# Optimization experiments

Measured on AMD Instinct MI355X. Metric: run time of the kernel, lower is better.

## Reference

```python
import jax, jax.numpy as jnp
import numpy as np

NEG_SLOPE = 0.01  # torch F.leaky_relu default

N_NODES = 100000
N_EDGES = 1250000
N_REL = 10
D = 64


def setup_inputs() -> dict:
    key = jax.random.key(0)
    ks = jax.random.split(key, 8)
    return {
        "nfeat": jax.random.normal(ks[0], (N_NODES, D), dtype=jnp.float32),
        "efeat": jax.random.normal(ks[1], (N_EDGES, D), dtype=jnp.float32),
        "relation_weight": jax.random.normal(ks[2], (N_REL, D, D), dtype=jnp.float32) * (1.0 / np.sqrt(D)),
        "res_fc_w": jax.random.normal(ks[3], (D, D), dtype=jnp.float32) * (1.0 / np.sqrt(D)),
        "res_fc2_w": jax.random.normal(ks[4], (D, D), dtype=jnp.float32) * (1.0 / np.sqrt(D)),
        "src": jax.random.randint(ks[5], (N_EDGES,), 0, N_NODES, dtype=jnp.int32),
        "dst": jnp.sort(jax.random.randint(ks[6], (N_EDGES,), 0, N_NODES, dtype=jnp.int32)),
        "etype": jax.random.randint(ks[7], (N_EDGES,), 0, N_REL, dtype=jnp.int32),
    }


def reference(nfeat, efeat, relation_weight, res_fc_w, res_fc2_w, src, dst, etype):
    # KGAT conv (eval mode, feat_drop=0):
    #   t_r = W_{r(e)} h_src,  h_r = W_{r(e)} h_dst
    #   att = <t_r, tanh(h_r + e_r)>  per edge
    #   a   = edge_softmax over incoming edges of dst
    #   h_neighbor[v] = sum_{e: dst=v} a_e * h_src
    #   h' = leaky_relu((h + h_nb) W1^T) + leaky_relu((h * h_nb) W2^T)
    n = nfeat.shape[0]
    # Project every node by every relation once (N*R*D), instead of
    # materializing a per-edge [E, D, D] weight gather.
    proj = jnp.einsum('ni,rio->nro', nfeat, relation_weight)  # [N, R, D]
    t_r = proj[src, etype]   # [E, D]
    h_r = proj[dst, etype]   # [E, D]
    att = jnp.sum(t_r * jnp.tanh(h_r + efeat), axis=-1)  # [E]

    # segment softmax over dst (edge_softmax)
    seg_max = jax.ops.segment_max(att, dst, num_segments=n)  # [N]
    ex = jnp.exp(att - seg_max[dst])
    seg_sum = jax.ops.segment_sum(ex, dst, num_segments=n)   # [N]
    a = ex / seg_sum[dst]                                    # [E]

    # weighted scatter-sum aggregation of src features
    h_nb = jax.ops.segment_sum(nfeat[src] * a[:, None], dst, num_segments=n)  # [N, D]

    out = (jax.nn.leaky_relu((nfeat + h_nb) @ res_fc_w.T, NEG_SLOPE)
           + jax.nn.leaky_relu((nfeat * h_nb) @ res_fc2_w.T, NEG_SLOPE))
    return out
```

## Files before the change

### kernel.cpp

```cpp
#include <hip/hip_runtime.h>
#include <hip/hip_fp16.h>
#include <math.h>

#define D 64
#define WAVE 64

typedef _Float16 f16;
typedef f16 f16x8 __attribute__((ext_vector_type(8)));
typedef float f32x4 __attribute__((ext_vector_type(4)));

__device__ __forceinline__ float wave_reduce_sum(float v) {
    v += __shfl_xor(v, 32);
    v += __shfl_xor(v, 16);
    v += __shfl_xor(v, 8);
    v += __shfl_xor(v, 4);
    v += __shfl_xor(v, 2);
    v += __shfl_xor(v, 1);
    return v;
}

__device__ __forceinline__ float wave_reduce_max(float v) {
    v = fmaxf(v, __shfl_xor(v, 32));
    v = fmaxf(v, __shfl_xor(v, 16));
    v = fmaxf(v, __shfl_xor(v, 8));
    v = fmaxf(v, __shfl_xor(v, 4));
    v = fmaxf(v, __shfl_xor(v, 2));
    v = fmaxf(v, __shfl_xor(v, 1));
    return v;
}

__device__ __forceinline__ float fast_tanh(float x) {
    float e = __expf(2.0f * x);
    return 1.0f - 2.0f / (e + 1.0f);
}

__global__ void wt_kernel(const float* __restrict__ W, f16* __restrict__ WT,
                          int n_rel) {
    int idx = blockIdx.x * blockDim.x + threadIdx.x;
    if (idx >= n_rel * D * D) return;
    int r = idx >> 12;
    int rem = idx & 4095;
    int o = rem >> 6;
    int k = rem & 63;
    WT[idx] = (f16)W[((size_t)r << 12) + (k << 6) + o];
}

__global__ __launch_bounds__(256) void proj_kernel(
    const float* __restrict__ nfeat, const f16* __restrict__ WT,
    f16* __restrict__ proj, int n_nodes, int n_rel) {
    __shared__ f16 Al[64 * D];
    const int tid = threadIdx.x;
    const int lane = tid & 63;
    const int wid = tid >> 6;
    const int n0 = blockIdx.x * 64;

    {
        const float4* g4 = (const float4*)(nfeat + (size_t)n0 * D);
        int avail_rows = n_nodes - n0;
        if (avail_rows > 64) avail_rows = 64;
        const int avail4 = avail_rows * (D / 4);
#pragma unroll
        for (int i = tid; i < 64 * (D / 4); i += 256) {
            float4 v = (i < avail4) ? g4[i] : make_float4(0.f, 0.f, 0.f, 0.f);
            f16* dp = &Al[i * 4];
            dp[0] = (f16)v.x; dp[1] = (f16)v.y; dp[2] = (f16)v.z; dp[3] = (f16)v.w;
        }
    }
    __syncthreads();

    const int g = lane >> 4;
    const int c = lane & 15;
    const int arow = wid * 16 + c;
    f16x8 a0 = *(const f16x8*)&Al[arow * D + g * 8];
    f16x8 a1 = *(const f16x8*)&Al[arow * D + 32 + g * 8];

    const int row_base = n0 + wid * 16 + g * 4;

    for (int r = 0; r < n_rel; ++r) {
        const f16* Wb = WT + ((size_t)r << 12);
        f32x4 acc[4] = {{0.f,0.f,0.f,0.f},{0.f,0.f,0.f,0.f},
                        {0.f,0.f,0.f,0.f},{0.f,0.f,0.f,0.f}};
#pragma unroll
        for (int t = 0; t < 4; ++t) {
            const f16* bp = Wb + (size_t)(t * 16 + c) * D + g * 8;
            f16x8 b0 = *(const f16x8*)bp;
            f16x8 b1 = *(const f16x8*)(bp + 32);
            acc[t] = __builtin_amdgcn_mfma_f32_16x16x32_f16(a0, b0, acc[t], 0, 0, 0);
            acc[t] = __builtin_amdgcn_mfma_f32_16x16x32_f16(a1, b1, acc[t], 0, 0, 0);
        }
#pragma unroll
        for (int t = 0; t < 4; ++t) {
#pragma unroll
            for (int j = 0; j < 4; ++j) {
                int n = row_base + j;
                if (n < n_nodes)
                    proj[((size_t)n * n_rel + r) * D + t * 16 + c] = (f16)acc[t][j];
            }
        }
    }
}

__global__ __launch_bounds__(256) void att_kernel(
    const __half* __restrict__ proj, const float* __restrict__ efeat,
    const int* __restrict__ src, const int* __restrict__ dst,
    const int* __restrict__ etype, float* __restrict__ att,
    int n_edges, int n_rel) {
    const int lane = threadIdx.x & 63;
    const int wid = threadIdx.x >> 6;
    const int g = lane >> 4;
    const int c4 = lane & 15;

    int e = (blockIdx.x * 4 + wid) * 4 + g;
    const bool valid = e < n_edges;
    const int ec = valid ? e : (n_edges - 1);
    const int s = src[ec];
    const int d = dst[ec];
    const int et = etype[ec];

    const float4* ef4 = (const float4*)(efeat + (size_t)ec * D);
    float4 ef = ef4[c4];
    const __half2* tp = (const __half2*)(proj + ((size_t)s * n_rel + et) * D) + c4 * 2;
    const __half2* hp = (const __half2*)(proj + ((size_t)d * n_rel + et) * D) + c4 * 2;
    float2 tA = __half22float2(tp[0]);
    float2 tB = __half22float2(tp[1]);
    float2 hA = __half22float2(hp[0]);
    float2 hB = __half22float2(hp[1]);

    float v = tA.x * fast_tanh(hA.x + ef.x)
            + tA.y * fast_tanh(hA.y + ef.y)
            + tB.x * fast_tanh(hB.x + ef.z)
            + tB.y * fast_tanh(hB.y + ef.w);
    v += __shfl_xor(v, 8);
    v += __shfl_xor(v, 4);
    v += __shfl_xor(v, 2);
    v += __shfl_xor(v, 1);
    if (valid && c4 == 0) att[e] = v;
}

__global__ void rowptr_kernel(const int* __restrict__ dst, int* __restrict__ row_ptr,
                              int n_edges, int n_nodes) {
    int tid = blockIdx.x * blockDim.x + threadIdx.x;
    int stride = gridDim.x * blockDim.x;
    for (int e = tid; e < n_edges; e += stride) {
        int d = dst[e];
        int dprev = (e == 0) ? -1 : dst[e - 1];
        for (int v = dprev + 1; v <= d; ++v) row_ptr[v] = e;
    }
    if (tid == 0) {
        int dlast = dst[n_edges - 1];
        for (int v = dlast + 1; v <= n_nodes; ++v) row_ptr[v] = n_edges;
    }
}

__global__ __launch_bounds__(256) void agg_kernel(
    const float* __restrict__ att, const int* __restrict__ src,
    const int* __restrict__ row_ptr, const float* __restrict__ nfeat,
    float* __restrict__ h_nb, int n_nodes) {
    const int lane = threadIdx.x & 63;
    const int wid = __builtin_amdgcn_readfirstlane(threadIdx.x >> 6);
    const int n = blockIdx.x * 4 + wid;
    if (n >= n_nodes) return;
    const int s = row_ptr[n];
    const int t = row_ptr[n + 1];
    float a0 = 0.0f, a1 = 0.0f, a2 = 0.0f, a3 = 0.0f;
    float inv = 0.0f;
    if (t > s) {
        float m = -INFINITY;
        for (int base = s; base < t; base += WAVE) {
            int idx = base + lane;
            float a = (idx < t) ? att[idx] : -INFINITY;
            m = fmaxf(m, a);
        }
        m = wave_reduce_max(m);
        float exsum = 0.0f;
        for (int base = s; base < t; base += WAVE) {
            int idx = base + lane;
            float ex = (idx < t) ? __expf(att[idx] - m) : 0.0f;
            int sv = (idx < t) ? src[idx] : 0;
            exsum += ex;
            int cnt = t - base;
            if (cnt > WAVE) cnt = WAVE;
            int cnt4 = (cnt + 3) & ~3;
            for (int j = 0; j < cnt4; j += 4) {
                float c0 = __shfl(ex, j + 0); int s0 = __shfl(sv, j + 0);
                float c1 = __shfl(ex, j + 1); int s1 = __shfl(sv, j + 1);
                float c2 = __shfl(ex, j + 2); int s2 = __shfl(sv, j + 2);
                float c3 = __shfl(ex, j + 3); int s3 = __shfl(sv, j + 3);
                a0 = fmaf(c0, nfeat[(size_t)s0 * D + lane], a0);
                a1 = fmaf(c1, nfeat[(size_t)s1 * D + lane], a1);
                a2 = fmaf(c2, nfeat[(size_t)s2 * D + lane], a2);
                a3 = fmaf(c3, nfeat[(size_t)s3 * D + lane], a3);
            }
        }
        float ssum = wave_reduce_sum(exsum);
        inv = 1.0f / ssum;
    }
    h_nb[(size_t)n * D + lane] = ((a0 + a1) + (a2 + a3)) * inv;
}

__global__ __launch_bounds__(256) void out_kernel(
    const float* __restrict__ nfeat, const float* h_nb,
    const float* __restrict__ W1, const float* __restrict__ W2,
    float* out, int n_nodes) {
    const int lane = threadIdx.x & 63;
    const int wid = __builtin_amdgcn_readfirstlane(threadIdx.x >> 6);
    float w1[D], w2[D];
#pragma unroll
    for (int i = 0; i < D; ++i) w1[i] = W1[lane * D + i];
#pragma unroll
    for (int i = 0; i < D; ++i) w2[i] = W2[lane * D + i];
    const int nwaves = gridDim.x * 4;
    for (int n = blockIdx.x * 4 + wid; n < n_nodes; n += nwaves) {
        const int nn = __builtin_amdgcn_readfirstlane(n);
        const float* x = nfeat + (size_t)nn * D;
        const float* h = h_nb + (size_t)nn * D;
        float a0 = 0.0f, a1 = 0.0f, b0 = 0.0f, b1 = 0.0f;
#pragma unroll
        for (int i = 0; i < D; i += 2) {
            float x0 = x[i], h0 = h[i];
            float x1 = x[i + 1], h1 = h[i + 1];
            a0 = fmaf(x0 + h0, w1[i], a0);
            b0 = fmaf(x0 * h0, w2[i], b0);
            a1 = fmaf(x1 + h1, w1[i + 1], a1);
            b1 = fmaf(x1 * h1, w2[i + 1], b1);
        }
        float a = a0 + a1, b = b0 + b1;
        a = (a > 0.0f) ? a : 0.01f * a;
        b = (b > 0.0f) ? b : 0.01f * b;
        out[(size_t)nn * D + lane] = a + b;
    }
}

extern "C" void kernel_launch(void* const* d_in, const int* in_sizes, int n_in,
                              void* d_out, int out_size, void* d_ws, size_t ws_size,
                              hipStream_t stream) {
    const float* nfeat = (const float*)d_in[0];
    const float* efeat = (const float*)d_in[1];
    const float* relw  = (const float*)d_in[2];
    const float* w1    = (const float*)d_in[3];
    const float* w2    = (const float*)d_in[4];
    const int*   src   = (const int*)d_in[5];
    const int*   dst   = (const int*)d_in[6];
    const int*   etype = (const int*)d_in[7];
    float* out = (float*)d_out;

    const int n_nodes = in_sizes[0] / D;
    const int n_edges = in_sizes[5];
    const int n_rel   = in_sizes[2] / (D * D);

    const size_t ALIGN = 256;
    const size_t proj_bytes = ((size_t)n_nodes * n_rel * D * sizeof(f16) + ALIGN - 1) & ~(ALIGN - 1);
    const size_t att_bytes  = ((size_t)n_edges * sizeof(float) + ALIGN - 1) & ~(ALIGN - 1);
    const size_t rp_bytes   = ((size_t)(n_nodes + 1) * sizeof(int) + ALIGN - 1) & ~(ALIGN - 1);

    float* h_nb = out;

    char* ws = (char*)d_ws;
    f16*  proj    = (f16*)ws;
    float* att    = (float*)(ws + proj_bytes);
    int* row_ptr  = (int*)(ws + proj_bytes + att_bytes);
    f16*  wt      = (f16*)(ws + proj_bytes + att_bytes + rp_bytes);

    rowptr_kernel<<<1024, 256, 0, stream>>>(dst, row_ptr, n_edges, n_nodes);

    wt_kernel<<<(n_rel * D * D + 255) / 256, 256, 0, stream>>>(relw, wt, n_rel);

    proj_kernel<<<(n_nodes + 63) / 64, 256, 0, stream>>>(nfeat, wt, proj,
                                                         n_nodes, n_rel);

    att_kernel<<<(n_edges + 15) / 16, 256, 0, stream>>>((const __half*)proj, efeat,
                                                        src, dst, etype,
                                                        att, n_edges, n_rel);

    agg_kernel<<<(n_nodes + 3) / 4, 256, 0, stream>>>(att, src, row_ptr, nfeat,
                                                      h_nb, n_nodes);

    out_kernel<<<1024, 256, 0, stream>>>(nfeat, h_nb, w1, w2, out, n_nodes);
}
```

Before: 695.4 us.

## Use fp16 node features for aggregation, widen edge/gather unrolling, nontemporal efeat loads

The projection kernel now also writes an fp16 copy of the node features, and the aggregation kernel gathers from it, halving gather bytes. The gather loop is unrolled to eight neighbours in flight. The attention kernel processes two edges per 16-lane group and loads edge features with nontemporal hints, and the output kernel grid grows to 3200 blocks. These changes cut memory traffic and raise memory-level parallelism, at the cost of reduced precision in the neighbour sum and extra workspace.

```diff
diff --git a/kernel.cpp b/kernel.cpp
--- a/kernel.cpp
+++ b/kernel.cpp
@@ -8,6 +8,7 @@
 typedef _Float16 f16;
 typedef f16 f16x8 __attribute__((ext_vector_type(8)));
 typedef float f32x4 __attribute__((ext_vector_type(4)));
+typedef float fv4 __attribute__((ext_vector_type(4)));
 
 __device__ __forceinline__ float wave_reduce_sum(float v) {
     v += __shfl_xor(v, 32);
@@ -47,7 +48,7 @@
 
 __global__ __launch_bounds__(256) void proj_kernel(
     const float* __restrict__ nfeat, const f16* __restrict__ WT,
-    f16* __restrict__ proj, int n_nodes, int n_rel) {
+    f16* __restrict__ proj, f16* __restrict__ nf16, int n_nodes, int n_rel) {
     __shared__ f16 Al[64 * D];
     const int tid = threadIdx.x;
     const int lane = tid & 63;
@@ -62,8 +63,13 @@
 #pragma unroll
         for (int i = tid; i < 64 * (D / 4); i += 256) {
             float4 v = (i < avail4) ? g4[i] : make_float4(0.f, 0.f, 0.f, 0.f);
+            f16 h0 = (f16)v.x, h1 = (f16)v.y, h2 = (f16)v.z, h3 = (f16)v.w;
             f16* dp = &Al[i * 4];
-            dp[0] = (f16)v.x; dp[1] = (f16)v.y; dp[2] = (f16)v.z; dp[3] = (f16)v.w;
+            dp[0] = h0; dp[1] = h1; dp[2] = h2; dp[3] = h3;
+            if (i < avail4) {
+                f16* np = nf16 + (size_t)n0 * D + i * 4;
+                np[0] = h0; np[1] = h1; np[2] = h2; np[3] = h3;
+            }
         }
     }
     __syncthreads();
@@ -110,31 +116,41 @@
     const int g = lane >> 4;
     const int c4 = lane & 15;
 
-    int e = (blockIdx.x * 4 + wid) * 4 + g;
-    const bool valid = e < n_edges;
-    const int ec = valid ? e : (n_edges - 1);
-    const int s = src[ec];
-    const int d = dst[ec];
-    const int et = etype[ec];
-
-    const float4* ef4 = (const float4*)(efeat + (size_t)ec * D);
-    float4 ef = ef4[c4];
-    const __half2* tp = (const __half2*)(proj + ((size_t)s * n_rel + et) * D) + c4 * 2;
-    const __half2* hp = (const __half2*)(proj + ((size_t)d * n_rel + et) * D) + c4 * 2;
-    float2 tA = __half22float2(tp[0]);
-    float2 tB = __half22float2(tp[1]);
-    float2 hA = __half22float2(hp[0]);
-    float2 hB = __half22float2(hp[1]);
-
-    float v = tA.x * fast_tanh(hA.x + ef.x)
-            + tA.y * fast_tanh(hA.y + ef.y)
-            + tB.x * fast_tanh(hB.x + ef.z)
-            + tB.y * fast_tanh(hB.y + ef.w);
-    v += __shfl_xor(v, 8);
-    v += __shfl_xor(v, 4);
-    v += __shfl_xor(v, 2);
-    v += __shfl_xor(v, 1);
-    if (valid && c4 == 0) att[e] = v;
+    const int eb = (blockIdx.x * 4 + wid) * 8 + g;
+    const int e0 = eb, e1 = eb + 4;
+    const bool v0 = e0 < n_edges, v1 = e1 < n_edges;
+    const int ec0 = v0 ? e0 : (n_edges - 1);
+    const int ec1 = v1 ? e1 : (n_edges - 1);
+    const int s0 = src[ec0], d0 = dst[ec0], t0 = etype[ec0];
+    const int s1 = src[ec1], d1 = dst[ec1], t1 = etype[ec1];
+
+    fv4 ef0 = __builtin_nontemporal_load((const fv4*)(efeat + (size_t)ec0 * D) + c4);
+    fv4 ef1 = __builtin_nontemporal_load((const fv4*)(efeat + (size_t)ec1 * D) + c4);
+    const __half2* tp0 = (const __half2*)(proj + ((size_t)s0 * n_rel + t0) * D) + c4 * 2;
+    const __half2* hp0 = (const __half2*)(proj + ((size_t)d0 * n_rel + t0) * D) + c4 * 2;
+    const __half2* tp1 = (const __half2*)(proj + ((size_t)s1 * n_rel + t1) * D) + c4 * 2;
+    const __half2* hp1 = (const __half2*)(proj + ((size_t)d1 * n_rel + t1) * D) + c4 * 2;
+    float2 tA0 = __half22float2(tp0[0]), tB0 = __half22float2(tp0[1]);
+    float2 hA0 = __half22float2(hp0[0]), hB0 = __half22float2(hp0[1]);
+    float2 tA1 = __half22float2(tp1[0]), tB1 = __half22float2(tp1[1]);
+    float2 hA1 = __half22float2(hp1[0]), hB1 = __half22float2(hp1[1]);
+
+    float r0 = tA0.x * fast_tanh(hA0.x + ef0.x)
+             + tA0.y * fast_tanh(hA0.y + ef0.y)
+             + tB0.x * fast_tanh(hB0.x + ef0.z)
+             + tB0.y * fast_tanh(hB0.y + ef0.w);
+    float r1 = tA1.x * fast_tanh(hA1.x + ef1.x)
+             + tA1.y * fast_tanh(hA1.y + ef1.y)
+             + tB1.x * fast_tanh(hB1.x + ef1.z)
+             + tB1.y * fast_tanh(hB1.y + ef1.w);
+    r0 += __shfl_xor(r0, 8); r1 += __shfl_xor(r1, 8);
+    r0 += __shfl_xor(r0, 4); r1 += __shfl_xor(r1, 4);
+    r0 += __shfl_xor(r0, 2); r1 += __shfl_xor(r1, 2);
+    r0 += __shfl_xor(r0, 1); r1 += __shfl_xor(r1, 1);
+    if (c4 == 0) {
+        if (v0) att[e0] = r0;
+        if (v1) att[e1] = r1;
+    }
 }
 
 __global__ void rowptr_kernel(const int* __restrict__ dst, int* __restrict__ row_ptr,
@@ -154,7 +170,7 @@
 
 __global__ __launch_bounds__(256) void agg_kernel(
     const float* __restrict__ att, const int* __restrict__ src,
-    const int* __restrict__ row_ptr, const float* __restrict__ nfeat,
+    const int* __restrict__ row_ptr, const f16* __restrict__ nf16,
     float* __restrict__ h_nb, int n_nodes) {
     const int lane = threadIdx.x & 63;
     const int wid = __builtin_amdgcn_readfirstlane(threadIdx.x >> 6);
@@ -162,7 +178,8 @@
     if (n >= n_nodes) return;
     const int s = row_ptr[n];
     const int t = row_ptr[n + 1];
-    float a0 = 0.0f, a1 = 0.0f, a2 = 0.0f, a3 = 0.0f;
+    float a0 = 0.f, a1 = 0.f, a2 = 0.f, a3 = 0.f;
+    float a4 = 0.f, a5 = 0.f, a6 = 0.f, a7 = 0.f;
     float inv = 0.0f;
     if (t > s) {
         float m = -INFINITY;
@@ -180,22 +197,31 @@
             exsum += ex;
             int cnt = t - base;
             if (cnt > WAVE) cnt = WAVE;
-            int cnt4 = (cnt + 3) & ~3;
-            for (int j = 0; j < cnt4; j += 4) {
+            int cnt8 = (cnt + 7) & ~7;
+            for (int j = 0; j < cnt8; j += 8) {
                 float c0 = __shfl(ex, j + 0); int s0 = __shfl(sv, j + 0);
                 float c1 = __shfl(ex, j + 1); int s1 = __shfl(sv, j + 1);
                 float c2 = __shfl(ex, j + 2); int s2 = __shfl(sv, j + 2);
                 float c3 = __shfl(ex, j + 3); int s3 = __shfl(sv, j + 3);
-                a0 = fmaf(c0, nfeat[(size_t)s0 * D + lane], a0);
-                a1 = fmaf(c1, nfeat[(size_t)s1 * D + lane], a1);
-                a2 = fmaf(c2, nfeat[(size_t)s2 * D + lane], a2);
-                a3 = fmaf(c3, nfeat[(size_t)s3 * D + lane], a3);
+                float c4 = __shfl(ex, j + 4); int s4 = __shfl(sv, j + 4);
+                float c5 = __shfl(ex, j + 5); int s5 = __shfl(sv, j + 5);
+                float c6 = __shfl(ex, j + 6); int s6 = __shfl(sv, j + 6);
+                float c7 = __shfl(ex, j + 7); int s7 = __shfl(sv, j + 7);
+                a0 = fmaf(c0, (float)nf16[(size_t)s0 * D + lane], a0);
+                a1 = fmaf(c1, (float)nf16[(size_t)s1 * D + lane], a1);
+                a2 = fmaf(c2, (float)nf16[(size_t)s2 * D + lane], a2);
+                a3 = fmaf(c3, (float)nf16[(size_t)s3 * D + lane], a3);
+                a4 = fmaf(c4, (float)nf16[(size_t)s4 * D + lane], a4);
+                a5 = fmaf(c5, (float)nf16[(size_t)s5 * D + lane], a5);
+                a6 = fmaf(c6, (float)nf16[(size_t)s6 * D + lane], a6);
+                a7 = fmaf(c7, (float)nf16[(size_t)s7 * D + lane], a7);
             }
         }
         float ssum = wave_reduce_sum(exsum);
         inv = 1.0f / ssum;
     }
-    h_nb[(size_t)n * D + lane] = ((a0 + a1) + (a2 + a3)) * inv;
+    h_nb[(size_t)n * D + lane] =
+        (((a0 + a1) + (a2 + a3)) + ((a4 + a5) + (a6 + a7))) * inv;
 }
 
 __global__ __launch_bounds__(256) void out_kernel(
@@ -252,6 +278,7 @@
     const size_t proj_bytes = ((size_t)n_nodes * n_rel * D * sizeof(f16) + ALIGN - 1) & ~(ALIGN - 1);
     const size_t att_bytes  = ((size_t)n_edges * sizeof(float) + ALIGN - 1) & ~(ALIGN - 1);
     const size_t rp_bytes   = ((size_t)(n_nodes + 1) * sizeof(int) + ALIGN - 1) & ~(ALIGN - 1);
+    const size_t wt_bytes   = ((size_t)n_rel * D * D * sizeof(f16) + ALIGN - 1) & ~(ALIGN - 1);
 
     float* h_nb = out;
 
@@ -260,20 +287,21 @@
     float* att    = (float*)(ws + proj_bytes);
     int* row_ptr  = (int*)(ws + proj_bytes + att_bytes);
     f16*  wt      = (f16*)(ws + proj_bytes + att_bytes + rp_bytes);
+    f16*  nf16    = (f16*)(ws + proj_bytes + att_bytes + rp_bytes + wt_bytes);
 
     rowptr_kernel<<<1024, 256, 0, stream>>>(dst, row_ptr, n_edges, n_nodes);
 
     wt_kernel<<<(n_rel * D * D + 255) / 256, 256, 0, stream>>>(relw, wt, n_rel);
 
-    proj_kernel<<<(n_nodes + 63) / 64, 256, 0, stream>>>(nfeat, wt, proj,
+    proj_kernel<<<(n_nodes + 63) / 64, 256, 0, stream>>>(nfeat, wt, proj, nf16,
                                                          n_nodes, n_rel);
 
-    att_kernel<<<(n_edges + 15) / 16, 256, 0, stream>>>((const __half*)proj, efeat,
+    att_kernel<<<(n_edges + 31) / 32, 256, 0, stream>>>((const __half*)proj, efeat,
                                                         src, dst, etype,
                                                         att, n_edges, n_rel);
 
-    agg_kernel<<<(n_nodes + 3) / 4, 256, 0, stream>>>(att, src, row_ptr, nfeat,
+    agg_kernel<<<(n_nodes + 3) / 4, 256, 0, stream>>>(att, src, row_ptr, nf16,
                                                       h_nb, n_nodes);
 
-    out_kernel<<<1024, 256, 0, stream>>>(nfeat, h_nb, w1, w2, out, n_nodes);
-}
+    out_kernel<<<3200, 256, 0, stream>>>(nfeat, h_nb, w1, w2, out, n_nodes);
+}
```

Result: no change. 691.4 us (-0.6%).
